# Optimization experiments

Measured on AMD Instinct MI355X. Metric: run time of the kernel, lower is better.

Reference implementation:

```python
import jax, jax.numpy as jnp
import numpy as np

D_MODEL = 2048
NUM_EXPERTS = 64
TOP_K = 2


def setup_inputs() -> dict:
    key = jax.random.key(0)
    k1, k2 = jax.random.split(key)
    x = jax.random.normal(k1, (4, 4096, D_MODEL), dtype=jnp.float32)
    # nn.Linear(d_model, num_experts) weight: [num_experts, d_model]
    W_gate = jax.random.normal(k2, (NUM_EXPERTS, D_MODEL), dtype=jnp.float32) * (1.0 / np.sqrt(D_MODEL))
    return {"x": x, "W_gate": W_gate}


def reference(x, W_gate):
    # logits: [b, s, e]
    logits = jnp.einsum("bsd,ed->bse", x, W_gate)
    probs = jax.nn.softmax(logits, axis=-1)
    expert_weights, expert_indices = jax.lax.top_k(probs, TOP_K)  # [b, s, k]
    expert_weights = expert_weights / jnp.sum(expert_weights, axis=-1, keepdims=True)
    return expert_indices, expert_weights
```

## Files before the change

### kernel.cpp

```cpp
#include <hip/hip_runtime.h>
#include <math.h>

#define NTOK 16384
#define DK   2048
#define NEXP 64

typedef float f32x4 __attribute__((ext_vector_type(4)));
typedef int   i32x4 __attribute__((ext_vector_type(4)));
typedef short s16x8 __attribute__((ext_vector_type(8)));

__device__ __forceinline__ unsigned short f2bf(float f) {
    union { float f; unsigned u; } v; v.f = f;
    unsigned r = (v.u + 0x7FFFu + ((v.u >> 16) & 1u)) >> 16;
    return (unsigned short)r;
}
__device__ __forceinline__ float bf2f(unsigned short h) {
    union { unsigned u; float f; } v; v.u = ((unsigned)h) << 16;
    return v.f;
}

__global__ __launch_bounds__(256) void wsplit_pack(const float* __restrict__ Wg,
                                                   unsigned short* __restrict__ ws) {
    const int t  = blockIdx.x * 256 + threadIdx.x;
    const int e  = t >> 8;
    const int k  = (t & 255) * 8;
    const int w  = k >> 9;
    const int c  = (k >> 5) & 15;
    const int g  = (k >> 3) & 3;
    const int rr = e & 15;
    const int n  = e >> 4;
    const int lane = g * 16 + rr;

    const float* src = Wg + (size_t)e * DK + k;
    unsigned short p0[8], p1[8], p2[8];
    #pragma unroll
    for (int j = 0; j < 8; ++j) {
        const float f = src[j];
        p0[j] = f2bf(f);  const float r1 = f - bf2f(p0[j]);
        p1[j] = f2bf(r1); const float r2 = r1 - bf2f(p1[j]);
        p2[j] = f2bf(r2);
    }
    const size_t base = ((((size_t)w * 16 + c) * 4 + n) * 3) * 512 + (size_t)lane * 8;
    *(s16x8*)(ws + base)        = *(s16x8*)p0;
    *(s16x8*)(ws + base + 512)  = *(s16x8*)p1;
    *(s16x8*)(ws + base + 1024) = *(s16x8*)p2;
}

__device__ __forceinline__ unsigned cvtpk(float lo, float hi) {
    unsigned r;
    asm("v_cvt_pk_bf16_f32 %0, %1, %2" : "=v"(r) : "v"(lo), "v"(hi));
    return r;
}

#define SPLIT2(F0, F1, O0, O1, O2) { \
    const unsigned q0 = cvtpk((F0), (F1)); \
    const float s0 = (F0) - __builtin_bit_cast(float, q0 << 16); \
    const float s1 = (F1) - __builtin_bit_cast(float, q0 & 0xFFFF0000u); \
    const unsigned q1 = cvtpk(s0, s1); \
    const float t0 = s0 - __builtin_bit_cast(float, q1 << 16); \
    const float t1 = s1 - __builtin_bit_cast(float, q1 & 0xFFFF0000u); \
    O0 = (int)q0; O1 = (int)q1; O2 = (int)cvtpk(t0, t1); }

#define ISSUE_X(XS, c) { \
    _Pragma("unroll") for (int m = 0; m < 2; ++m) \
        _Pragma("unroll") for (int h = 0; h < 2; ++h) \
            XS[m][h] = *(const float4*)(xbase + (size_t)m * 16 * DK + h * 4 + (c) * 32); }

#define ISSUE_B(BS, c) { \
    _Pragma("unroll") for (int n = 0; n < 4; ++n) \
        _Pragma("unroll") for (int p = 0; p < 3; ++p) \
            BS[n][p] = *(const i32x4*)(wbase + ((size_t)(c) * 12 + n * 3 + p) * 512); }

#define CONV1(XS, m) { \
    SPLIT2(XS[m][0].x, XS[m][0].y, A[m][0].x, A[m][1].x, A[m][2].x); \
    SPLIT2(XS[m][0].z, XS[m][0].w, A[m][0].y, A[m][1].y, A[m][2].y); \
    SPLIT2(XS[m][1].x, XS[m][1].y, A[m][0].z, A[m][1].z, A[m][2].z); \
    SPLIT2(XS[m][1].z, XS[m][1].w, A[m][0].w, A[m][1].w, A[m][2].w); }

#define MFMA_TERM(pa, pb, BS) { \
    _Pragma("unroll") for (int m = 0; m < 2; ++m) \
        _Pragma("unroll") for (int n = 0; n < 4; ++n) \
            acc[m][n] = __builtin_amdgcn_mfma_f32_16x16x32_bf16( \
                __builtin_bit_cast(s16x8, A[m][pa]), \
                __builtin_bit_cast(s16x8, BS[n][pb]), acc[m][n], 0, 0, 0); }

#define MFMA_ALL(BS) \
    MFMA_TERM(0, 0, BS) MFMA_TERM(0, 1, BS) MFMA_TERM(1, 0, BS) \
    MFMA_TERM(1, 1, BS) MFMA_TERM(0, 2, BS) MFMA_TERM(2, 0, BS)

#define PHASE(XS, BS, c, NCNT, DO_ISSUE) { \
    asm volatile("s_waitcnt vmcnt(" #NCNT ")" ::: "memory"); \
    __builtin_amdgcn_sched_barrier(0); \
    CONV1(XS, 0); CONV1(XS, 1); \
    MFMA_ALL(BS); \
    if (DO_ISSUE) { ISSUE_X(XS, (c) + 3); ISSUE_B(BS, (c) + 3); } \
    __builtin_amdgcn_sched_barrier(0); }

__global__ __launch_bounds__(256, 2) void topk_router_kernel(
    const float* __restrict__ x,
    const unsigned short* __restrict__ ws,
    float* __restrict__ out)
{
    __shared__ float lg[4][32][68];

    const int tid  = threadIdx.x;
    const int w    = tid >> 6;
    const int lane = tid & 63;
    const int rr   = lane & 15;
    const int g    = lane >> 4;
    const int tok0 = blockIdx.x * 32;

    const float* xbase = x + (size_t)(tok0 + rr) * DK + w * 512 + g * 8;
    const unsigned short* wbase = ws + (size_t)w * 98304 + (size_t)lane * 8;

    f32x4 acc[2][4];
    #pragma unroll
    for (int m = 0; m < 2; ++m)
        #pragma unroll
        for (int n = 0; n < 4; ++n) acc[m][n] = (f32x4){0.f, 0.f, 0.f, 0.f};

    float4 X0[2][2], X1[2][2], X2[2][2];
    i32x4  B0[4][3], B1[4][3], B2[4][3];
    i32x4  A[2][3];

    ISSUE_X(X0, 0); ISSUE_B(B0, 0);
    ISSUE_X(X1, 1); ISSUE_B(B1, 1);
    ISSUE_X(X2, 2); ISSUE_B(B2, 2);

    #pragma unroll 1
    for (int c = 0; c < 12; c += 3) {
        PHASE(X0, B0, c + 0, 32, 1);
        PHASE(X1, B1, c + 1, 32, 1);
        PHASE(X2, B2, c + 2, 32, 1);
    }
    PHASE(X0, B0, 12, 32, 1);
    PHASE(X1, B1, 13, 32, 0);
    PHASE(X2, B2, 14, 16, 0);
    PHASE(X0, B0, 15,  0, 0);

    #pragma unroll
    for (int m = 0; m < 2; ++m)
        #pragma unroll
        for (int n = 0; n < 4; ++n)
            #pragma unroll
            for (int r = 0; r < 4; ++r)
                lg[w][m * 16 + g * 4 + r][n * 16 + rr] = acc[m][n][r];
    __syncthreads();

    #pragma unroll 1
    for (int t = 0; t < 8; ++t) {
        const int tok = w * 8 + t;
        const float v = lg[0][tok][lane] + lg[1][tok][lane]
                      + lg[2][tok][lane] + lg[3][tok][lane];

        float m1 = v; int i1 = lane;
        #pragma unroll
        for (int off = 32; off > 0; off >>= 1) {
            float ov = __shfl_xor(m1, off);
            int   oi = __shfl_xor(i1, off);
            if (ov > m1 || (ov == m1 && oi < i1)) { m1 = ov; i1 = oi; }
        }
        float m2 = (lane == i1) ? -INFINITY : v; int i2 = lane;
        #pragma unroll
        for (int off = 32; off > 0; off >>= 1) {
            float ov = __shfl_xor(m2, off);
            int   oi = __shfl_xor(i2, off);
            if (ov > m2 || (ov == m2 && oi < i2)) { m2 = ov; i2 = oi; }
        }

        if (lane == 0) {
            const int gtok = tok0 + tok;
            const float e  = expf(m2 - m1);
            const float w1 = 1.0f / (1.0f + e);
            const float w2 = e / (1.0f + e);
            out[gtok * 2 + 0] = (float)i1;
            out[gtok * 2 + 1] = (float)i2;
            out[NTOK * 2 + gtok * 2 + 0] = w1;
            out[NTOK * 2 + gtok * 2 + 1] = w2;
        }
    }
}

extern "C" void kernel_launch(void* const* d_in, const int* in_sizes, int n_in,
                              void* d_out, int out_size, void* d_ws, size_t ws_size,
                              hipStream_t stream) {
    const float* x  = (const float*)d_in[0];
    const float* Wg = (const float*)d_in[1];
    float* out = (float*)d_out;
    unsigned short* ws = (unsigned short*)d_ws;
    hipLaunchKernelGGL(wsplit_pack, dim3(64), dim3(256), 0, stream, Wg, ws);
    hipLaunchKernelGGL(topk_router_kernel, dim3(NTOK / 32), dim3(256), 0, stream,
                       x, ws, out);
}
```

Measured before the change: 50.89 us.

## Split-K GEMM with LDS-staged weights and separate top-k reduce kernel

Each block now covers 128 tokens over one 256-wide slice of K (split-K by 8) instead of 32 tokens over full K. The packed bf16x3 weights are staged into shared memory with global_load_lds and triple buffering, so the four waves share them rather than each loading its own copy. Partial logits go to a workspace and a new reduce kernel sums them and does the top-2 selection. The aim is more weight reuse and better occupancy (launch bounds go to 3 blocks), at the cost of an extra kernel launch and extra global traffic for the partial sums.

New measurement: 64.30 us. +26.3%, slower.

```diff
diff --git a/kernel.cpp b/kernel.cpp
--- a/kernel.cpp
+++ b/kernel.cpp
@@ -24,8 +24,7 @@
     const int t  = blockIdx.x * 256 + threadIdx.x;
     const int e  = t >> 8;
     const int k  = (t & 255) * 8;
-    const int w  = k >> 9;
-    const int c  = (k >> 5) & 15;
+    const int R  = k >> 5;
     const int g  = (k >> 3) & 3;
     const int rr = e & 15;
     const int n  = e >> 4;
@@ -40,10 +39,16 @@
         p1[j] = f2bf(r1); const float r2 = r1 - bf2f(p1[j]);
         p2[j] = f2bf(r2);
     }
-    const size_t base = ((((size_t)w * 16 + c) * 4 + n) * 3) * 512 + (size_t)lane * 8;
+    const size_t base = (((size_t)R * 4 + n) * 3) * 512 + (size_t)lane * 8;
     *(s16x8*)(ws + base)        = *(s16x8*)p0;
     *(s16x8*)(ws + base + 512)  = *(s16x8*)p1;
     *(s16x8*)(ws + base + 1024) = *(s16x8*)p2;
+}
+
+__device__ __forceinline__ void gload_lds16(const float* src, float* dst) {
+    __builtin_amdgcn_global_load_lds(
+        (const __attribute__((address_space(1))) void*)src,
+        (__attribute__((address_space(3))) void*)dst, 16, 0, 0);
 }
 
 __device__ __forceinline__ unsigned cvtpk(float lo, float hi) {
@@ -66,10 +71,11 @@
         _Pragma("unroll") for (int h = 0; h < 2; ++h) \
             XS[m][h] = *(const float4*)(xbase + (size_t)m * 16 * DK + h * 4 + (c) * 32); }
 
-#define ISSUE_B(BS, c) { \
-    _Pragma("unroll") for (int n = 0; n < 4; ++n) \
-        _Pragma("unroll") for (int p = 0; p < 3; ++p) \
-            BS[n][p] = *(const i32x4*)(wbase + ((size_t)(c) * 12 + n * 3 + p) * 512); }
+#define STAGE_B(c, BUF) { \
+    _Pragma("unroll") for (int j = 0; j < 3; ++j) { \
+        const int f = w3 + j; \
+        gload_lds16(wsf + ((size_t)(R0 + (c)) * 12 + f) * 256 + lane4, \
+                    &bB[BUF][f * 256]); } }
 
 #define CONV1(XS, m) { \
     SPLIT2(XS[m][0].x, XS[m][0].y, A[m][0].x, A[m][1].x, A[m][2].x); \
@@ -77,41 +83,52 @@
     SPLIT2(XS[m][1].x, XS[m][1].y, A[m][0].z, A[m][1].z, A[m][2].z); \
     SPLIT2(XS[m][1].z, XS[m][1].w, A[m][0].w, A[m][1].w, A[m][2].w); }
 
-#define MFMA_TERM(pa, pb, BS) { \
-    _Pragma("unroll") for (int m = 0; m < 2; ++m) \
-        _Pragma("unroll") for (int n = 0; n < 4; ++n) \
-            acc[m][n] = __builtin_amdgcn_mfma_f32_16x16x32_bf16( \
-                __builtin_bit_cast(s16x8, A[m][pa]), \
-                __builtin_bit_cast(s16x8, BS[n][pb]), acc[m][n], 0, 0, 0); }
-
-#define MFMA_ALL(BS) \
-    MFMA_TERM(0, 0, BS) MFMA_TERM(0, 1, BS) MFMA_TERM(1, 0, BS) \
-    MFMA_TERM(1, 1, BS) MFMA_TERM(0, 2, BS) MFMA_TERM(2, 0, BS)
-
-#define PHASE(XS, BS, c, NCNT, DO_ISSUE) { \
+#define MFMA1(Aa, Bb, Cc) __builtin_amdgcn_mfma_f32_16x16x32_bf16( \
+    __builtin_bit_cast(s16x8, Aa), __builtin_bit_cast(s16x8, Bb), Cc, 0, 0, 0)
+
+#define MFMA_N(n, BUF) { \
+    const i32x4 bn0 = *(const i32x4*)&bB[BUF][((n) * 3 + 0) * 256 + lane4]; \
+    const i32x4 bn1 = *(const i32x4*)&bB[BUF][((n) * 3 + 1) * 256 + lane4]; \
+    const i32x4 bn2 = *(const i32x4*)&bB[BUF][((n) * 3 + 2) * 256 + lane4]; \
+    _Pragma("unroll") for (int m = 0; m < 2; ++m) { \
+        acc[m][n] = MFMA1(A[m][0], bn0, acc[m][n]); \
+        acc[m][n] = MFMA1(A[m][0], bn1, acc[m][n]); \
+        acc[m][n] = MFMA1(A[m][1], bn0, acc[m][n]); \
+        acc[m][n] = MFMA1(A[m][1], bn1, acc[m][n]); \
+        acc[m][n] = MFMA1(A[m][0], bn2, acc[m][n]); \
+        acc[m][n] = MFMA1(A[m][2], bn0, acc[m][n]); } }
+
+#define ROUND(c, XS, BUF, NCNT, DO_ISSUE, NBUF) { \
     asm volatile("s_waitcnt vmcnt(" #NCNT ")" ::: "memory"); \
     __builtin_amdgcn_sched_barrier(0); \
+    __builtin_amdgcn_s_barrier(); \
+    __builtin_amdgcn_sched_barrier(0); \
     CONV1(XS, 0); CONV1(XS, 1); \
-    MFMA_ALL(BS); \
-    if (DO_ISSUE) { ISSUE_X(XS, (c) + 3); ISSUE_B(BS, (c) + 3); } \
+    MFMA_N(0, BUF) MFMA_N(1, BUF) MFMA_N(2, BUF) MFMA_N(3, BUF) \
+    if (DO_ISSUE) { STAGE_B((c) + 2, NBUF); ISSUE_X(XS, (c) + 2); } \
     __builtin_amdgcn_sched_barrier(0); }
 
-__global__ __launch_bounds__(256, 2) void topk_router_kernel(
+__global__ __launch_bounds__(256, 3) void topk_gemm(
     const float* __restrict__ x,
     const unsigned short* __restrict__ ws,
-    float* __restrict__ out)
+    float* __restrict__ part)
 {
-    __shared__ float lg[4][32][68];
+    __shared__ float bB[3][3072];
 
     const int tid  = threadIdx.x;
     const int w    = tid >> 6;
     const int lane = tid & 63;
     const int rr   = lane & 15;
     const int g    = lane >> 4;
-    const int tok0 = blockIdx.x * 32;
-
-    const float* xbase = x + (size_t)(tok0 + rr) * DK + w * 512 + g * 8;
-    const unsigned short* wbase = ws + (size_t)w * 98304 + (size_t)lane * 8;
+    const int w3   = w * 3;
+    const int lane4 = lane * 4;
+    const int tg   = blockIdx.x >> 3;
+    const int ks   = blockIdx.x & 7;
+    const int R0   = ks * 8;
+    const int tok0 = tg * 128 + w * 32;
+    const float* wsf = (const float*)ws;
+
+    const float* xbase = x + (size_t)(tok0 + rr) * DK + ks * 256 + g * 8;
 
     f32x4 acc[2][4];
     #pragma unroll
@@ -119,39 +136,48 @@
         #pragma unroll
         for (int n = 0; n < 4; ++n) acc[m][n] = (f32x4){0.f, 0.f, 0.f, 0.f};
 
-    float4 X0[2][2], X1[2][2], X2[2][2];
-    i32x4  B0[4][3], B1[4][3], B2[4][3];
+    float4 X0[2][2], X1[2][2];
     i32x4  A[2][3];
 
-    ISSUE_X(X0, 0); ISSUE_B(B0, 0);
-    ISSUE_X(X1, 1); ISSUE_B(B1, 1);
-    ISSUE_X(X2, 2); ISSUE_B(B2, 2);
-
-    #pragma unroll 1
-    for (int c = 0; c < 12; c += 3) {
-        PHASE(X0, B0, c + 0, 32, 1);
-        PHASE(X1, B1, c + 1, 32, 1);
-        PHASE(X2, B2, c + 2, 32, 1);
-    }
-    PHASE(X0, B0, 12, 32, 1);
-    PHASE(X1, B1, 13, 32, 0);
-    PHASE(X2, B2, 14, 16, 0);
-    PHASE(X0, B0, 15,  0, 0);
-
+    STAGE_B(0, 0); ISSUE_X(X0, 0);
+    STAGE_B(1, 1); ISSUE_X(X1, 1);
+
+    ROUND(0, X0, 0, 7, 1, 2);
+    ROUND(1, X1, 1, 7, 1, 0);
+    ROUND(2, X0, 2, 7, 1, 1);
+    ROUND(3, X1, 0, 7, 1, 2);
+    ROUND(4, X0, 1, 7, 1, 0);
+    ROUND(5, X1, 2, 7, 1, 1);
+    ROUND(6, X0, 0, 7, 0, 0);
+    ROUND(7, X1, 1, 0, 0, 0);
+
+    float* pbase = part + ((size_t)ks << 20);
     #pragma unroll
     for (int m = 0; m < 2; ++m)
         #pragma unroll
         for (int n = 0; n < 4; ++n)
             #pragma unroll
             for (int r = 0; r < 4; ++r)
-                lg[w][m * 16 + g * 4 + r][n * 16 + rr] = acc[m][n][r];
-    __syncthreads();
+                pbase[(size_t)(tok0 + m * 16 + g * 4 + r) * 64 + n * 16 + rr]
+                    = acc[m][n][r];
+}
+
+__global__ __launch_bounds__(256) void topk_reduce(
+    const float* __restrict__ part,
+    float* __restrict__ out)
+{
+    const int tid  = threadIdx.x;
+    const int wv   = tid >> 6;
+    const int lane = tid & 63;
+    const int tokb = blockIdx.x * 64 + wv * 16;
 
     #pragma unroll 1
-    for (int t = 0; t < 8; ++t) {
-        const int tok = w * 8 + t;
-        const float v = lg[0][tok][lane] + lg[1][tok][lane]
-                      + lg[2][tok][lane] + lg[3][tok][lane];
+    for (int t = 0; t < 16; ++t) {
+        const int tok = tokb + t;
+        float v = 0.f;
+        #pragma unroll
+        for (int s = 0; s < 8; ++s)
+            v += part[((size_t)s << 20) + (size_t)tok * 64 + lane];
 
         float m1 = v; int i1 = lane;
         #pragma unroll
@@ -169,14 +195,13 @@
         }
 
         if (lane == 0) {
-            const int gtok = tok0 + tok;
             const float e  = expf(m2 - m1);
             const float w1 = 1.0f / (1.0f + e);
             const float w2 = e / (1.0f + e);
-            out[gtok * 2 + 0] = (float)i1;
-            out[gtok * 2 + 1] = (float)i2;
-            out[NTOK * 2 + gtok * 2 + 0] = w1;
-            out[NTOK * 2 + gtok * 2 + 1] = w2;
+            out[tok * 2 + 0] = (float)i1;
+            out[tok * 2 + 1] = (float)i2;
+            out[NTOK * 2 + tok * 2 + 0] = w1;
+            out[NTOK * 2 + tok * 2 + 1] = w2;
         }
     }
 }
@@ -188,7 +213,9 @@
     const float* Wg = (const float*)d_in[1];
     float* out = (float*)d_out;
     unsigned short* ws = (unsigned short*)d_ws;
+    float* part = (float*)((char*)d_ws + (1 << 20));
+
     hipLaunchKernelGGL(wsplit_pack, dim3(64), dim3(256), 0, stream, Wg, ws);
-    hipLaunchKernelGGL(topk_router_kernel, dim3(NTOK / 32), dim3(256), 0, stream,
-                       x, ws, out);
-}
+    hipLaunchKernelGGL(topk_gemm, dim3(1024), dim3(256), 0, stream, x, ws, part);
+    hipLaunchKernelGGL(topk_reduce, dim3(256), dim3(256), 0, stream, part, out);
+}
```

## Stage x tiles through LDS via global_load_lds with double-buffered pipeline

Applied to the files above, without the earlier changes.

Loads of x now go straight from global memory into shared memory with coalesced 16-byte global_load_lds transfers, where each wave stages its own 32x32 sub-tile. The fp32-to-bf16 split conversion then reads its operands back from LDS. The register pipeline drops from three stages to two, which frees VGPRs that previously held x and B prefetch buffers. This trades extra LDS traffic and a shallower prefetch depth for better global coalescing and lower register pressure, and the LDS region is reused for the logits after a barrier.

Result: faster. 47.87 us (-5.9%).

```diff
diff --git a/kernel.cpp b/kernel.cpp
--- a/kernel.cpp
+++ b/kernel.cpp
@@ -46,6 +46,12 @@
     *(s16x8*)(ws + base + 1024) = *(s16x8*)p2;
 }
 
+__device__ __forceinline__ void gload_lds16(const float* src, float* dst) {
+    __builtin_amdgcn_global_load_lds(
+        (const __attribute__((address_space(1))) void*)src,
+        (__attribute__((address_space(3))) void*)dst, 16, 0, 0);
+}
+
 __device__ __forceinline__ unsigned cvtpk(float lo, float hi) {
     unsigned r;
     asm("v_cvt_pk_bf16_f32 %0, %1, %2" : "=v"(r) : "v"(lo), "v"(hi));
@@ -61,21 +67,24 @@
     const float t1 = s1 - __builtin_bit_cast(float, q1 & 0xFFFF0000u); \
     O0 = (int)q0; O1 = (int)q1; O2 = (int)cvtpk(t0, t1); }
 
-#define ISSUE_X(XS, c) { \
-    _Pragma("unroll") for (int m = 0; m < 2; ++m) \
-        _Pragma("unroll") for (int h = 0; h < 2; ++h) \
-            XS[m][h] = *(const float4*)(xbase + (size_t)m * 16 * DK + h * 4 + (c) * 32); }
+#define STAGE_X(c, BUF) { \
+    _Pragma("unroll") for (int it = 0; it < 4; ++it) \
+        gload_lds16(xsrc + (size_t)it * 8 * DK + (size_t)(c) * 32, \
+                    &xs[w][BUF][it * 256]); }
 
 #define ISSUE_B(BS, c) { \
     _Pragma("unroll") for (int n = 0; n < 4; ++n) \
         _Pragma("unroll") for (int p = 0; p < 3; ++p) \
             BS[n][p] = *(const i32x4*)(wbase + ((size_t)(c) * 12 + n * 3 + p) * 512); }
 
-#define CONV1(XS, m) { \
-    SPLIT2(XS[m][0].x, XS[m][0].y, A[m][0].x, A[m][1].x, A[m][2].x); \
-    SPLIT2(XS[m][0].z, XS[m][0].w, A[m][0].y, A[m][1].y, A[m][2].y); \
-    SPLIT2(XS[m][1].x, XS[m][1].y, A[m][0].z, A[m][1].z, A[m][2].z); \
-    SPLIT2(XS[m][1].z, XS[m][1].w, A[m][0].w, A[m][1].w, A[m][2].w); }
+#define CONV_LDS(BUF) { \
+    _Pragma("unroll") for (int m = 0; m < 2; ++m) { \
+        const float4 xa0 = *(const float4*)&xs[w][BUF][(rr + 16 * m) * 32 + g * 8]; \
+        const float4 xa1 = *(const float4*)&xs[w][BUF][(rr + 16 * m) * 32 + g * 8 + 4]; \
+        SPLIT2(xa0.x, xa0.y, A[m][0].x, A[m][1].x, A[m][2].x); \
+        SPLIT2(xa0.z, xa0.w, A[m][0].y, A[m][1].y, A[m][2].y); \
+        SPLIT2(xa1.x, xa1.y, A[m][0].z, A[m][1].z, A[m][2].z); \
+        SPLIT2(xa1.z, xa1.w, A[m][0].w, A[m][1].w, A[m][2].w); } }
 
 #define MFMA_TERM(pa, pb, BS) { \
     _Pragma("unroll") for (int m = 0; m < 2; ++m) \
@@ -88,12 +97,12 @@
     MFMA_TERM(0, 0, BS) MFMA_TERM(0, 1, BS) MFMA_TERM(1, 0, BS) \
     MFMA_TERM(1, 1, BS) MFMA_TERM(0, 2, BS) MFMA_TERM(2, 0, BS)
 
-#define PHASE(XS, BS, c, NCNT, DO_ISSUE) { \
+#define PHASE(BS, c, NCNT, DO_ISSUE) { \
     asm volatile("s_waitcnt vmcnt(" #NCNT ")" ::: "memory"); \
     __builtin_amdgcn_sched_barrier(0); \
-    CONV1(XS, 0); CONV1(XS, 1); \
+    CONV_LDS((c) & 1); \
     MFMA_ALL(BS); \
-    if (DO_ISSUE) { ISSUE_X(XS, (c) + 3); ISSUE_B(BS, (c) + 3); } \
+    if (DO_ISSUE) { STAGE_X((c) + 2, (c) & 1); ISSUE_B(BS, (c) + 2); } \
     __builtin_amdgcn_sched_barrier(0); }
 
 __global__ __launch_bounds__(256, 2) void topk_router_kernel(
@@ -101,7 +110,9 @@
     const unsigned short* __restrict__ ws,
     float* __restrict__ out)
 {
-    __shared__ float lg[4][32][68];
+    __shared__ float smem[8704];
+    float (*xs)[2][1024] = (float (*)[2][1024])smem;
+    float (*lg)[32][68]  = (float (*)[32][68])smem;
 
     const int tid  = threadIdx.x;
     const int w    = tid >> 6;
@@ -110,7 +121,9 @@
     const int g    = lane >> 4;
     const int tok0 = blockIdx.x * 32;
 
-    const float* xbase = x + (size_t)(tok0 + rr) * DK + w * 512 + g * 8;
+    const int lt = lane >> 3;
+    const int lq = lane & 7;
+    const float* xsrc = x + (size_t)(tok0 + lt) * DK + w * 512 + lq * 4;
     const unsigned short* wbase = ws + (size_t)w * 98304 + (size_t)lane * 8;
 
     f32x4 acc[2][4];
@@ -119,25 +132,21 @@
         #pragma unroll
         for (int n = 0; n < 4; ++n) acc[m][n] = (f32x4){0.f, 0.f, 0.f, 0.f};
 
-    float4 X0[2][2], X1[2][2], X2[2][2];
-    i32x4  B0[4][3], B1[4][3], B2[4][3];
-    i32x4  A[2][3];
-
-    ISSUE_X(X0, 0); ISSUE_B(B0, 0);
-    ISSUE_X(X1, 1); ISSUE_B(B1, 1);
-    ISSUE_X(X2, 2); ISSUE_B(B2, 2);
+    i32x4 B0[4][3], B1[4][3];
+    i32x4 A[2][3];
+
+    STAGE_X(0, 0); ISSUE_B(B0, 0);
+    STAGE_X(1, 1); ISSUE_B(B1, 1);
 
     #pragma unroll 1
-    for (int c = 0; c < 12; c += 3) {
-        PHASE(X0, B0, c + 0, 32, 1);
-        PHASE(X1, B1, c + 1, 32, 1);
-        PHASE(X2, B2, c + 2, 32, 1);
+    for (int c = 0; c < 14; c += 2) {
+        PHASE(B0, c,     16, 1);
+        PHASE(B1, c + 1, 16, 1);
     }
-    PHASE(X0, B0, 12, 32, 1);
-    PHASE(X1, B1, 13, 32, 0);
-    PHASE(X2, B2, 14, 16, 0);
-    PHASE(X0, B0, 15,  0, 0);
-
+    PHASE(B0, 14, 16, 0);
+    PHASE(B1, 15,  0, 0);
+
+    __syncthreads();
     #pragma unroll
     for (int m = 0; m < 2; ++m)
         #pragma unroll
```
